# Performance work log

Hardware: AMD Instinct MI355X
Metric: run time of the kernel (lower is better)

Reference implementation:

```python
import jax, jax.numpy as jnp
import numpy as np

# q_config constants
W_IN, E_IN = 8, 4          # data_in_width, data_in_exponent_width
R_W = 6                     # data_r_width
W_OUT, E_OUT = 8, 4        # data_out_width, data_out_exponent_width (= data_n_width)
EXP_SUM_UF = 4              # exp_sum_underflow_bits
DIV_UF = 4                  # division_underflow_bits
W_DATA, E_DATA = 8, 4      # data_width, data_exponent_width

N, D = 8192, 2048


def integer_quantizer(x, width, frac_width):
    s = 2.0 ** frac_width
    lo, hi = -(2.0 ** (width - 1)), 2.0 ** (width - 1) - 1
    return jnp.clip(jnp.round(x * s), lo, hi) / s


def integer_floor_quantizer(x, width, frac_width):
    s = 2.0 ** frac_width
    lo, hi = -(2.0 ** (width - 1)), 2.0 ** (width - 1) - 1
    return jnp.clip(jnp.floor(x * s), lo, hi) / s


def mxint_quant(x, width, exponent_width):
    # MXInt block quantization with parallelism [1,1]: per-element shared exponent.
    e_hi, e_lo = 2.0 ** (exponent_width - 1) - 1, -(2.0 ** (exponent_width - 1))
    ax = jnp.abs(x)
    e = jnp.ceil(jnp.log2(jnp.where(ax == 0, 1.0, ax)))
    e = jnp.clip(e, e_lo, e_hi)
    scale = 2.0 ** (width - 1)
    m = jnp.clip(jnp.round(x * 2.0 ** (-e) * scale), -scale, scale - 1)
    qx = m * 2.0 ** e / scale
    return qx, m, e


def setup_inputs() -> dict:
    key = jax.random.key(0)
    x = jax.random.normal(key, (N, D), dtype=jnp.float32)
    return {"x": x}


def reference(x):
    # ---- MXIntHardwareExp: quantize input, range-reduce x = r + n*ln2 ----
    qx, _, _ = mxint_quant(x, W_IN, E_IN)
    log2e, _, _ = mxint_quant(jnp.float32(np.log2(np.e)), 8, 4)
    y = qx * log2e
    y = integer_floor_quantizer(y, E_OUT + R_W - 1, R_W - 1)
    n = jnp.floor(y)
    r = y - n                                # r in [0, 1)
    mexp = integer_quantizer(2.0 ** r, W_OUT, W_OUT - 2) * 2.0 ** (W_OUT - 2)
    eexp = n                                 # qexp = mexp * 2^eexp / 2^(W_OUT-2)

    # ---- exp_sum: exponent-aligned integer accumulation over dim 1 ----
    ms = (mexp * 2.0 ** EXP_SUM_UF).T        # [D, N]
    es = eexp.T                              # [D, N]

    def step(carry, me):
        out, emax = carry
        mi, ei = me
        new_emax = jnp.maximum(emax, ei)
        out = jnp.floor(out * 2.0 ** (emax - new_emax)) + jnp.floor(mi * 2.0 ** (ei - new_emax))
        return (out, new_emax), None

    (mexp_sum, eexp_sum), _ = jax.lax.scan(step, (ms[0], es[0]), (ms[1:], es[1:]))
    # mexp_sum, eexp_sum: [N]

    # ---- division: per-element mantissa integer division by the sum ----
    mout = jnp.floor(mexp * 2.0 ** (DIV_UF + EXP_SUM_UF) / mexp_sum[:, None])
    eout = eexp - eexp_sum[:, None]
    qout = mout * 2.0 ** eout / 2.0 ** DIV_UF
    qout, _, _ = mxint_quant(qout, W_DATA, E_DATA)
    return qout
```

## Files before the change

kernel.cpp:

```cpp
#include <hip/hip_runtime.h>


#define D_DIM 2048
#define TPB   256
#define EPT   8

__device__ __constant__ int c_mexp_tab[32] = {
    64, 65, 67, 68, 70, 71, 73, 74, 76, 78, 79, 81, 83, 85, 87, 89,
    91, 92, 95, 97, 99, 101, 103, 105, 108, 110, 112, 115, 117, 120, 123, 125
};

__global__ __launch_bounds__(TPB) void mxint_softmax_kernel(const float* __restrict__ x,
                                                            float* __restrict__ out) {
    const int t    = threadIdx.x;
    const int row  = blockIdx.x;
    const int lane = t & 63;
    const int wid  = t >> 6;

    __shared__ int       s_tab[32];
    __shared__ int       s_wmax[4];
    __shared__ long long s_wsum[4];

    if (t < 32) s_tab[t] = c_mexp_tab[t];
    __syncthreads();

    const size_t base = (size_t)row * D_DIM + (size_t)t * EPT;
    const float4 v0 = *(const float4*)(x + base);
    const float4 v1 = *(const float4*)(x + base + 4);
    float xs[8] = {v0.x, v0.y, v0.z, v0.w, v1.x, v1.y, v1.z, v1.w};

    int me[8], ee[8], lp[8];
    int run = -1000;
#pragma unroll
    for (int j = 0; j < 8; ++j) {
        const float xv = xs[j];
        const unsigned bits  = __float_as_uint(xv) & 0x7fffffffu;
        const int      ebits = (int)(bits >> 23);
        const unsigned mant  = bits & 0x7fffffu;
        int e = (ebits == 0) ? -1000 : ((mant == 0) ? (ebits - 127) : (ebits - 126));
        e = min(7, max(-8, e));
        const float scale_up = __uint_as_float((unsigned)(7 - e + 127) << 23);
        float m = rintf(xv * scale_up);
        m = fminf(127.0f, fmaxf(-128.0f, m));
        const float scale_dn = __uint_as_float((unsigned)(e - 7 + 127) << 23);
        const float y32 = m * 46.0f * scale_dn;
        int yq = (int)floorf(y32);
        yq = min(255, max(-256, yq));
        ee[j] = yq >> 5;
        me[j] = s_tab[yq & 31];
        run   = max(run, ee[j]);
        lp[j] = run;
    }

    int v = run;
#pragma unroll
    for (int d = 1; d < 64; d <<= 1) {
        const int o = __shfl_up(v, d, 64);
        if (lane >= d) v = max(v, o);
    }
    if (lane == 63) s_wmax[wid] = v;
    __syncthreads();
    int wpref = -1000;
#pragma unroll
    for (int w = 0; w < 4; ++w)
        if (w < wid) wpref = max(wpref, s_wmax[w]);
    int excl_wave = __shfl_up(v, 1, 64);
    if (lane == 0) excl_wave = -1000;
    const int P = max(wpref, excl_wave);

    long long partial = 0;
#pragma unroll
    for (int j = 0; j < 8; ++j) {
        const int E  = max(P, lp[j]);
        const int sh = E - ee[j];
        const int c  = (me[j] << 4) >> sh;
        partial += (long long)c << (E + 8);
    }
#pragma unroll
    for (int d = 32; d >= 1; d >>= 1) partial += __shfl_down(partial, d, 64);
    if (lane == 0) s_wsum[wid] = partial;
    __syncthreads();

    const long long total = s_wsum[0] + s_wsum[1] + s_wsum[2] + s_wsum[3];
    const int Estar = max(max(s_wmax[0], s_wmax[1]), max(s_wmax[2], s_wmax[3]));
    const unsigned msum = (unsigned)(total >> (Estar + 8));

    float res[8];
#pragma unroll
    for (int j = 0; j < 8; ++j) {
        const unsigned mout = ((unsigned)me[j] << 8) / msum;
        float o = 0.0f;
        if (mout != 0u) {
            const int  eout = ee[j] - Estar;
            const int  bl   = 32 - __clz(mout);
            const bool pw2  = (mout & (mout - 1u)) == 0u;
            const int  clog = pw2 ? (bl - 1) : bl;
            const int  e2   = clog + eout - 4;
            int m2, e2c;
            if (e2 >= -8) {
                e2c = e2;
                m2  = pw2 ? 127 : (int)(mout << (7 - clog));
            } else {
                e2c = -8;
                const int sh = eout + 11;
                if (sh >= 0) {
                    m2 = (int)(mout << sh);
                } else {
                    const int      s2   = -sh;
                    const unsigned bse  = mout >> s2;
                    const unsigned frac = mout & ((1u << s2) - 1u);
                    const unsigned half = 1u << (s2 - 1);
                    m2 = (int)(bse + ((frac > half || (frac == half && (bse & 1u))) ? 1u : 0u));
                }
            }
            o = (float)m2 * __uint_as_float((unsigned)(e2c - 7 + 127) << 23);
        }
        res[j] = o;
    }

    float4 r0 = {res[0], res[1], res[2], res[3]};
    float4 r1 = {res[4], res[5], res[6], res[7]};
    *(float4*)(out + base)     = r0;
    *(float4*)(out + base + 4) = r1;
}

extern "C" void kernel_launch(void* const* d_in, const int* in_sizes, int n_in,
                              void* d_out, int out_size, void* d_ws, size_t ws_size,
                              hipStream_t stream) {
    const float* x   = (const float*)d_in[0];
    float*       out = (float*)d_out;
    const int rows = in_sizes[0] / D_DIM;
    mxint_softmax_kernel<<<rows, TPB, 0, stream>>>(x, out);
}
```

Baseline: 111.9 us.

## Replace per-element division with magic reciprocal and slim integer arithmetic paths

Rewrites the per-element compute. The lookup table now comes from a register via ds_bpermute instead of shared memory, which drops a __syncthreads. Mantissa and exponent are packed into one int, and the quantisation uses integer shifts. The partial sums use 32-bit arithmetic with a mixed 32/64-bit wave reduction, and each element's integer division becomes a multiply by a magic reciprocal computed once per row. The output requantisation is made branch-free. The kernel is likely memory-bound, so the ALU savings may not matter much, and the magic-division and 32-bit-sum changes risk exactness.

```diff
diff --git a/kernel.cpp b/kernel.cpp
--- a/kernel.cpp
+++ b/kernel.cpp
@@ -13,43 +13,36 @@
 __global__ __launch_bounds__(TPB) void mxint_softmax_kernel(const float* __restrict__ x,
                                                             float* __restrict__ out) {
     const int t    = threadIdx.x;
-    const int row  = blockIdx.x;
     const int lane = t & 63;
     const int wid  = t >> 6;
 
-    __shared__ int       s_tab[32];
-    __shared__ int       s_wmax[4];
-    __shared__ long long s_wsum[4];
+    __shared__ int                s_wmax[4];
+    __shared__ unsigned long long s_wsum[4];
 
-    if (t < 32) s_tab[t] = c_mexp_tab[t];
-    __syncthreads();
+    const int tv = c_mexp_tab[lane & 31];
 
-    const size_t base = (size_t)row * D_DIM + (size_t)t * EPT;
+    const size_t base = (size_t)blockIdx.x * D_DIM + (size_t)t * EPT;
     const float4 v0 = *(const float4*)(x + base);
     const float4 v1 = *(const float4*)(x + base + 4);
-    float xs[8] = {v0.x, v0.y, v0.z, v0.w, v1.x, v1.y, v1.z, v1.w};
+    const float xs[8] = {v0.x, v0.y, v0.z, v0.w, v1.x, v1.y, v1.z, v1.w};
 
-    int me[8], ee[8], lp[8];
-    int run = -1000;
+    int pk[8];
+    int run = -8;
 #pragma unroll
     for (int j = 0; j < 8; ++j) {
-        const float xv = xs[j];
-        const unsigned bits  = __float_as_uint(xv) & 0x7fffffffu;
-        const int      ebits = (int)(bits >> 23);
-        const unsigned mant  = bits & 0x7fffffu;
-        int e = (ebits == 0) ? -1000 : ((mant == 0) ? (ebits - 127) : (ebits - 126));
+        const float    xv   = xs[j];
+        const unsigned bits = __float_as_uint(xv) & 0x7fffffffu;
+        int e = (int)(bits >> 23) - 127 + (((bits & 0x7fffffu) != 0u) ? 1 : 0);
         e = min(7, max(-8, e));
-        const float scale_up = __uint_as_float((unsigned)(7 - e + 127) << 23);
-        float m = rintf(xv * scale_up);
-        m = fminf(127.0f, fmaxf(-128.0f, m));
-        const float scale_dn = __uint_as_float((unsigned)(e - 7 + 127) << 23);
-        const float y32 = m * 46.0f * scale_dn;
-        int yq = (int)floorf(y32);
+        const float su = __uint_as_float((unsigned)(134 - e) << 23);
+        int mi = (int)rintf(xv * su);
+        mi = min(127, max(-128, mi));
+        int yq = (mi * 46) >> (7 - e);
         yq = min(255, max(-256, yq));
-        ee[j] = yq >> 5;
-        me[j] = s_tab[yq & 31];
-        run   = max(run, ee[j]);
-        lp[j] = run;
+        const int ee = yq >> 5;
+        const int me = __builtin_amdgcn_ds_bpermute((yq & 31) << 2, tv);
+        pk[j] = me | ((ee + 8) << 8);
+        run   = max(run, ee);
     }
 
     int v = run;
@@ -60,75 +53,79 @@
     }
     if (lane == 63) s_wmax[wid] = v;
     __syncthreads();
-    int wpref = -1000;
+
+    int wpref = -8;
 #pragma unroll
     for (int w = 0; w < 4; ++w)
         if (w < wid) wpref = max(wpref, s_wmax[w]);
-    int excl_wave = __shfl_up(v, 1, 64);
-    if (lane == 0) excl_wave = -1000;
-    const int P = max(wpref, excl_wave);
+    int ex = __shfl_up(v, 1, 64);
+    if (lane == 0) ex = -8;
+    const int P = max(wpref, ex);
 
-    long long partial = 0;
+    unsigned partial = 0;
+    int E = P;
 #pragma unroll
     for (int j = 0; j < 8; ++j) {
-        const int E  = max(P, lp[j]);
-        const int sh = E - ee[j];
-        const int c  = (me[j] << 4) >> sh;
-        partial += (long long)c << (E + 8);
+        const int ee = (pk[j] >> 8) - 8;
+        const int me = pk[j] & 0xff;
+        E = max(E, ee);
+        const unsigned c = ((unsigned)me << 4) >> (E - ee);
+        partial += c << (E + 8);
     }
-#pragma unroll
-    for (int d = 32; d >= 1; d >>= 1) partial += __shfl_down(partial, d, 64);
-    if (lane == 0) s_wsum[wid] = partial;
+
+    unsigned p32 = partial;
+    p32 += __shfl_down(p32, 32, 64);
+    p32 += __shfl_down(p32, 16, 64);
+    p32 += __shfl_down(p32, 8, 64);
+    unsigned long long p64 = p32;
+    p64 += __shfl_down(p64, 4, 64);
+    p64 += __shfl_down(p64, 2, 64);
+    p64 += __shfl_down(p64, 1, 64);
+    if (lane == 0) s_wsum[wid] = p64;
     __syncthreads();
 
-    const long long total = s_wsum[0] + s_wsum[1] + s_wsum[2] + s_wsum[3];
+    const unsigned long long total = s_wsum[0] + s_wsum[1] + s_wsum[2] + s_wsum[3];
     const int Estar = max(max(s_wmax[0], s_wmax[1]), max(s_wmax[2], s_wmax[3]));
     const unsigned msum = (unsigned)(total >> (Estar + 8));
+
+    const unsigned mq    = 0x80000000u / msum;
+    const unsigned mr    = 0x80000000u - mq * msum;
+    const unsigned magic = (mq << 7) + ((mr << 7) / msum) + 1u;
 
     float res[8];
 #pragma unroll
     for (int j = 0; j < 8; ++j) {
-        const unsigned mout = ((unsigned)me[j] << 8) / msum;
-        float o = 0.0f;
-        if (mout != 0u) {
-            const int  eout = ee[j] - Estar;
-            const int  bl   = 32 - __clz(mout);
-            const bool pw2  = (mout & (mout - 1u)) == 0u;
-            const int  clog = pw2 ? (bl - 1) : bl;
-            const int  e2   = clog + eout - 4;
-            int m2, e2c;
-            if (e2 >= -8) {
-                e2c = e2;
-                m2  = pw2 ? 127 : (int)(mout << (7 - clog));
-            } else {
-                e2c = -8;
-                const int sh = eout + 11;
-                if (sh >= 0) {
-                    m2 = (int)(mout << sh);
-                } else {
-                    const int      s2   = -sh;
-                    const unsigned bse  = mout >> s2;
-                    const unsigned frac = mout & ((1u << s2) - 1u);
-                    const unsigned half = 1u << (s2 - 1);
-                    m2 = (int)(bse + ((frac > half || (frac == half && (bse & 1u))) ? 1u : 0u));
-                }
-            }
-            o = (float)m2 * __uint_as_float((unsigned)(e2c - 7 + 127) << 23);
-        }
-        res[j] = o;
+        const int      me   = pk[j] & 0xff;
+        const int      ee   = (pk[j] >> 8) - 8;
+        const unsigned num  = (unsigned)(me << 8);
+        const unsigned mout = (unsigned)(((unsigned long long)num * magic) >> 38);
+        const int eout = ee - Estar;
+        const int bl   = 32 - __clz((int)(mout | 1u));
+        const int pw2  = ((mout & (mout - 1u)) == 0u) ? 1 : 0;
+        const int clog = bl - pw2;
+        const int s    = min(7 - clog, eout + 11);
+        const int rs   = 8 - s;
+        const unsigned u    = mout << 8;
+        const unsigned bse  = u >> rs;
+        const unsigned frac = u & ((1u << rs) - 1u);
+        const unsigned half = 1u << (rs - 1);
+        unsigned m2 = bse + (((frac > half) || (frac == half && (bse & 1u))) ? 1u : 0u);
+        m2 = min(m2, 127u);
+        const int ef = max(clog + eout - 4, -8);
+        res[j] = (float)m2 * __uint_as_float((unsigned)(ef + 120) << 23);
     }
 
-    float4 r0 = {res[0], res[1], res[2], res[3]};
-    float4 r1 = {res[4], res[5], res[6], res[7]};
-    *(float4*)(out + base)     = r0;
-    *(float4*)(out + base + 4) = r1;
+    const float4 out0 = {res[0], res[1], res[2], res[3]};
+    const float4 out1 = {res[4], res[5], res[6], res[7]};
+    *(float4*)(out + base)     = out0;
+    *(float4*)(out + base + 4) = out1;
 }
 
 extern "C" void kernel_launch(void* const* d_in, const int* in_sizes, int n_in,
                               void* d_out, int out_size, void* d_ws, size_t ws_size,
                               hipStream_t stream) {
     const float* x   = (const float*)d_in[0];
-    float*       out = (float*)d_out;
+    float*       o   = (float*)d_out;
     const int rows = in_sizes[0] / D_DIM;
-    mxint_softmax_kernel<<<rows, TPB, 0, stream>>>(x, out);
+    mxint_softmax_kernel<<<rows, TPB, 0, stream>>>(x, o);
 }
```

After: 121.2 us. +8.3%, slower.
